# Performance work log

Measured on AMD Instinct MI355X. Metric: run time of the kernel, lower is better.

Reference implementation:

```python
import jax, jax.numpy as jnp
import numpy as np
from jax import lax

B0, H0, W0, C0 = 16, 32, 32, 512
D_ = C0 // 4      # per-group channels = d_inner (expand=1)
S = 1             # d_state
R = 8             # dt_rank = ceil(D_/16)


def layernorm(x, w, b, eps=1e-5):
    m = jnp.mean(x, axis=-1, keepdims=True)
    v = jnp.mean((x - m) ** 2, axis=-1, keepdims=True)
    return (x - m) / jnp.sqrt(v + eps) * w + b


def silu(x):
    return x * jax.nn.sigmoid(x)


def selective_scan(u, delta, A, Bs, Cs, Dp):
    # u,delta:(B,d,L)  A:(d,S)  Bs,Cs:(B,S,L)  Dp:(d,)
    a = jnp.exp(jnp.einsum('bdl,ds->bdsl', delta, A))      # decay per step
    bx = jnp.einsum('bdl,bsl,bdl->bdsl', delta, Bs, u)     # input injection
    def comb(c1, c2):
        a1, b1 = c1
        a2, b2 = c2
        return (a1 * a2, a2 * b1 + b2)
    _, h = lax.associative_scan(comb, (a, bx), axis=-1)    # h_t = a_t h_{t-1} + b_t
    return jnp.einsum('bdsl,bsl->bdl', h, Cs) + Dp[None, :, None] * u


def ss2d(xg, direction, ipw, cw, cb, xpw, dtw, dtb, Alog, Dp, onw, onb, opw):
    # xg: (B,H,W,dm); single-direction SS2D branch (CrossScan_i / CrossMerge_i)
    Bsz, Hh, Ww, dm = xg.shape
    xz = jnp.einsum('bhwc,oc->bhwo', xg, ipw)              # in_proj -> 2*d_inner
    xc, z = jnp.split(xz, 2, axis=-1)
    xc = xc.transpose(0, 3, 1, 2)                           # (B,d,H,W)
    xc = lax.conv_general_dilated(xc, cw, (1, 1), [(1, 1), (1, 1)],
                                  dimension_numbers=('NCHW', 'OIHW', 'NCHW'),
                                  feature_group_count=dm) + cb[None, :, None, None]
    xc = silu(xc)
    L = Hh * Ww
    if direction == 0:
        xs = xc.reshape(Bsz, dm, L)                         # row-major forward
    elif direction == 1:
        xs = xc.transpose(0, 1, 3, 2).reshape(Bsz, dm, L)   # column-major forward
    elif direction == 2:
        xs = xc.reshape(Bsz, dm, L)[:, :, ::-1]             # row-major reversed
    else:
        xs = xc.transpose(0, 1, 3, 2).reshape(Bsz, dm, L)[:, :, ::-1]
    xd = jnp.einsum('bdl,cd->bcl', xs, xpw)                 # x_proj -> (dt,B,C)
    dts, Bc, Cc = jnp.split(xd, [R, R + S], axis=1)
    delta = jax.nn.softplus(jnp.einsum('brl,dr->bdl', dts, dtw) + dtb[None, :, None])
    A = -jnp.exp(Alog)                                      # (d,S)
    y = selective_scan(xs, delta, A, Bc, Cc, Dp)
    if direction == 0:
        yhw = y.reshape(Bsz, dm, Hh, Ww)
    elif direction == 1:
        yhw = y.reshape(Bsz, dm, Ww, Hh).transpose(0, 1, 3, 2)
    elif direction == 2:
        yhw = y[:, :, ::-1].reshape(Bsz, dm, Hh, Ww)
    else:
        yhw = y[:, :, ::-1].reshape(Bsz, dm, Ww, Hh).transpose(0, 1, 3, 2)
    yo = yhw.transpose(0, 2, 3, 1)                          # (B,H,W,d)
    yo = layernorm(yo, onw, onb)
    yo = yo * silu(z)
    return jnp.einsum('bhwd,od->bhwo', yo, opw)             # out_proj


def setup_inputs() -> dict:
    key = jax.random.key(0)
    ks = jax.random.split(key, 12)
    def rn(k, shape, scale=0.02):
        return (jax.random.normal(k, shape) * scale).astype(jnp.float32)
    return dict(
        x=jax.random.normal(ks[0], (B0, H0 * W0, C0), dtype=jnp.float32),
        H=H0, W=W0,
        norm_w=jnp.ones((C0,), jnp.float32), norm_b=jnp.zeros((C0,), jnp.float32),
        fc_w=rn(ks[1], (C0, C0)), fc_b=jnp.zeros((C0,), jnp.float32),
        eca_w=rn(ks[2], (3,), 0.3),
        skip_scale=jnp.ones((), jnp.float32),
        proj_w=rn(ks[3], (C0, C0)), proj_b=jnp.zeros((C0,), jnp.float32),
        in_proj_w=rn(ks[4], (4, 2 * D_, D_)),
        conv_w=rn(ks[5], (4, D_, 1, 3, 3), 0.1), conv_b=jnp.zeros((4, D_), jnp.float32),
        x_proj_w=rn(ks[6], (4, R + 2 * S, D_)),
        dt_proj_w=rn(ks[7], (4, D_, R), 0.1), dt_proj_b=rn(ks[8], (4, D_), 0.1),
        A_log=jnp.zeros((4, D_, S), jnp.float32),           # A = -1 (d_state=1 init)
        D_param=jnp.ones((4, D_), jnp.float32),
        out_norm_w=jnp.ones((4, D_), jnp.float32), out_norm_b=jnp.zeros((4, D_), jnp.float32),
        out_proj_w=rn(ks[9], (4, D_, D_)),
    )


def reference(x, H, W, norm_w, norm_b, fc_w, fc_b, eca_w, skip_scale, proj_w, proj_b,
              in_proj_w, conv_w, conv_b, x_proj_w, dt_proj_w, dt_proj_b, A_log, D_param,
              out_norm_w, out_norm_b, out_proj_w):
    Bsz, N, Cc = x.shape
    xn = layernorm(x, norm_w, norm_b)
    # ECA-style channel gate: mean over tokens, 1D conv (k=3) over channel axis
    z_avg = jnp.mean(xn, axis=1)                            # (B,C)
    zp = jnp.pad(z_avg, ((0, 0), (1, 1)))
    y_eca = eca_w[0] * zp[:, :-2] + eca_w[1] * zp[:, 1:-1] + eca_w[2] * zp[:, 2:]
    gate = jax.nn.sigmoid(jnp.einsum('bc,oc->bo', z_avg, fc_w) + fc_b + y_eca)
    xh = xn.reshape(Bsz, H, W, Cc)
    groups = jnp.split(xh, 4, axis=-1)
    ys = []
    for g in range(4):                                      # 4 directional SS2D branches
        ys.append(ss2d(groups[g], g, in_proj_w[g], conv_w[g], conv_b[g], x_proj_w[g],
                       dt_proj_w[g], dt_proj_b[g], A_log[g], D_param[g],
                       out_norm_w[g], out_norm_b[g], out_proj_w[g]))
    xm = jnp.concatenate(ys, axis=-1) * skip_scale * xh
    xm = xm.reshape(Bsz, N, Cc) * gate[:, None, :]
    xm = layernorm(xm, norm_w, norm_b)
    return jnp.einsum('bnc,oc->bno', xm, proj_w) + proj_b
```

## Files before the change

kernel.cpp:

```cpp
#include <hip/hip_runtime.h>
#include <math.h>

#define NTOK 16384
#define NC 512
#define ND 128
#define NCH 64
#define CST 16

typedef __attribute__((ext_vector_type(8))) short bf16x8;
typedef __attribute__((ext_vector_type(4))) float f32x4;

#define LOG2E 1.4426950408889634f
#define LN2   0.6931471805599453f

__device__ __forceinline__ float fexp(float x){ return __builtin_amdgcn_exp2f(x * LOG2E); }
__device__ __forceinline__ float flog(float x){ return __builtin_amdgcn_logf(x) * LN2; }
__device__ __forceinline__ float sigf(float x){ return 1.f/(1.f + fexp(-x)); }

__device__ __forceinline__ float b2f(ushort u){ unsigned x = ((unsigned)u)<<16; return __builtin_bit_cast(float,x); }
__device__ __forceinline__ ushort f2b(float f){
  unsigned u = __builtin_bit_cast(unsigned,f);
  u += 0x7fff + ((u>>16)&1);
  return (ushort)(u>>16);
}

__device__ __forceinline__ int perm_pos(int g, int l){
  switch(g){
    case 0: return l;
    case 1: return ((l & 31) << 5) | (l >> 5);
    case 2: return 1023 - l;
    default:{ int ll = 1023 - l; return ((ll & 31) << 5) | (ll >> 5); }
  }
}

__device__ __forceinline__ void gload16(const void* g, void* l){
  __builtin_amdgcn_global_load_lds((const __attribute__((address_space(1))) void*)g,
                                   (__attribute__((address_space(3))) void*)l, 16, 0, 0);
}

__global__ __launch_bounds__(256) void k_tobf16_4(
    const float* __restrict__ s1, int n1, ushort* __restrict__ d1,
    const float* __restrict__ s2, int n2, ushort* __restrict__ d2,
    const float* __restrict__ s3, int n3, ushort* __restrict__ d3,
    const float* __restrict__ s4, int n4, ushort* __restrict__ d4){
  int i = blockIdx.x*256 + threadIdx.x;
  if (i < n1) d1[i] = f2b(s1[i]);
  else if (i < n1+n2) d2[i-n1] = f2b(s2[i-n1]);
  else if (i < n1+n2+n3) d3[i-n1-n2] = f2b(s3[i-n1-n2]);
  else if (i < n1+n2+n3+n4) d4[i-n1-n2-n3] = f2b(s4[i-n1-n2-n3]);
}

__global__ __launch_bounds__(256) void k_ln512(const float* __restrict__ x,
    const float* __restrict__ w, const float* __restrict__ b, ushort* __restrict__ out){
  int wv = threadIdx.x >> 6, lane = threadIdx.x & 63;
  int t = blockIdx.x*4 + wv;
  const float* xr = x + (size_t)t*NC + lane*8;
  float4 a = *(const float4*)xr;
  float4 c = *(const float4*)(xr+4);
  float e[8] = {a.x,a.y,a.z,a.w,c.x,c.y,c.z,c.w};
  float s = 0.f, sq = 0.f;
  #pragma unroll
  for (int i=0;i<8;i++){ s += e[i]; sq += e[i]*e[i]; }
  #pragma unroll
  for (int o=1;o<64;o<<=1){ s += __shfl_xor(s,o); sq += __shfl_xor(sq,o); }
  float m = s*(1.f/NC);
  float var = sq*(1.f/NC) - m*m;
  float rs = rsqrtf(var + 1e-5f);
  const float4* wr = (const float4*)(w + lane*8);
  const float4* br = (const float4*)(b + lane*8);
  float4 w0 = wr[0], w1 = wr[1], b0 = br[0], b1 = br[1];
  float wv8[8] = {w0.x,w0.y,w0.z,w0.w,w1.x,w1.y,w1.z,w1.w};
  float bv8[8] = {b0.x,b0.y,b0.z,b0.w,b1.x,b1.y,b1.z,b1.w};
  bf16x8 o8;
  #pragma unroll
  for (int i=0;i<8;i++) ((ushort*)&o8)[i] = f2b((e[i]-m)*rs*wv8[i]+bv8[i]);
  *(bf16x8*)(out + (size_t)t*NC + lane*8) = o8;
}

__global__ __launch_bounds__(512) void k_cm1(const ushort* __restrict__ xn,
    float* __restrict__ part){
  int c = threadIdx.x;
  const ushort* base = xn + ((size_t)blockIdx.x*32)*NC + c;
  float acc = 0.f;
  for (int n=0;n<32;n++) acc += b2f(base[(size_t)n*NC]);
  part[(size_t)blockIdx.x*NC + c] = acc;
}
__global__ __launch_bounds__(512) void k_cm2(const float* __restrict__ part,
    float* __restrict__ zavg){
  int b = blockIdx.x, c = threadIdx.x;
  float acc = 0.f;
  for (int i=0;i<32;i++) acc += part[(size_t)(b*32+i)*NC + c];
  zavg[b*NC+c] = acc * (1.f/1024.f);
}

__global__ __launch_bounds__(256) void k_gate(const float* __restrict__ zavg,
    const float* __restrict__ fcw, const float* __restrict__ fcb,
    const float* __restrict__ ew, float* __restrict__ gate){
  __shared__ float za[NC];
  int b = blockIdx.x >> 7, og = blockIdx.x & 127;
  int tid = threadIdx.x, lane = tid & 63, wv = tid >> 6;
  za[tid]     = zavg[b*NC + tid];
  za[tid+256] = zavg[b*NC + tid + 256];
  __syncthreads();
  int o = og*4 + wv;
  const float* wr = fcw + (size_t)o*NC;
  float acc = 0.f;
  #pragma unroll
  for (int i=0;i<8;i++) acc += za[lane + i*64]*wr[lane + i*64];
  #pragma unroll
  for (int off=1;off<64;off<<=1) acc += __shfl_xor(acc, off);
  if (lane==0){
    float left  = (o>0)    ? za[o-1] : 0.f;
    float right = (o<NC-1) ? za[o+1] : 0.f;
    float ye = ew[0]*left + ew[1]*za[o] + ew[2]*right;
    gate[b*NC+o] = sigf(acc + fcb[o] + ye);
  }
}

__global__ __launch_bounds__(256) void k_gemm_bf16(
    const ushort* __restrict__ A, int lda, long sAz,
    const ushort* __restrict__ Bw, int ldb, long sBz, int K,
    ushort* __restrict__ C0, int ldc0, ushort* __restrict__ C1, int ldc1,
    int nsplit, long sCz,
    float* __restrict__ Cf, int ldcf, const float* __restrict__ bias, int swz)
{
  __shared__ __align__(16) ushort Asm[128*64];
  __shared__ __align__(16) ushort Bsm[128*64];
  const int z = blockIdx.z;
  A  += (size_t)z*sAz;
  Bw += (size_t)z*sBz;
  if (C0) C0 += (size_t)z*sCz;
  if (C1) C1 += (size_t)z*sCz;
  int bx = blockIdx.x, by = blockIdx.y;
  if (swz){
    int nx = gridDim.x, nwg = nx * gridDim.y;
    int lin = by*nx + bx;
    int cpx = nwg >> 3;
    int s = (lin & 7)*cpx + (lin >> 3);
    bx = s % nx; by = s / nx;
  }
  const int tid = threadIdx.x;
  const int lane = tid & 63, wid = tid >> 6;
  const int wm = wid >> 1, wn = wid & 1;
  const int m0 = by * 128, n0 = bx * 128;

  const ushort* ga[4]; const ushort* gb[4]; int ldst[4];
  #pragma unroll
  for (int j=0;j<4;j++){
    int c = tid + 256*j;
    int r = c >> 3;
    int kb = ((c & 7) << 4) ^ ((r & 7) << 4);
    ga[j] = A  + (size_t)(m0 + r)*lda + (kb >> 1);
    gb[j] = Bw + (size_t)(n0 + r)*ldb + (kb >> 1);
    ldst[j] = c * 8;
  }

  f32x4 acc[4][4];
  #pragma unroll
  for (int i=0;i<4;i++)
    #pragma unroll
    for (int j=0;j<4;j++) acc[i][j] = (f32x4){0.f,0.f,0.f,0.f};

  const int lc = lane & 15;
  const int kgrp = (lane >> 4) << 4;

  for (int k0 = 0; k0 < K; k0 += 64){
    #pragma unroll
    for (int j=0;j<4;j++) gload16(ga[j] + k0, Asm + ldst[j]);
    #pragma unroll
    for (int j=0;j<4;j++) gload16(gb[j] + k0, Bsm + ldst[j]);
    __syncthreads();
    #pragma unroll
    for (int kk=0; kk<2; kk++){
      bf16x8 af[4], bfr[4];
      #pragma unroll
      for (int i=0;i<4;i++){
        int ra = wm*64 + i*16 + lc;
        int kb = kk*64 + kgrp;
        af[i] = *(const bf16x8*)((const char*)Asm + ra*128 + (kb ^ ((ra&7)<<4)));
        int rb = wn*64 + i*16 + lc;
        bfr[i] = *(const bf16x8*)((const char*)Bsm + rb*128 + (kb ^ ((rb&7)<<4)));
      }
      #pragma unroll
      for (int i=0;i<4;i++)
        #pragma unroll
        for (int j=0;j<4;j++)
          acc[i][j] = __builtin_amdgcn_mfma_f32_16x16x32_bf16(af[i], bfr[j], acc[i][j], 0, 0, 0);
    }
    __syncthreads();
  }

  const int lr = (lane >> 4) * 4;
  if (Cf){
    #pragma unroll
    for (int i=0;i<4;i++)
      #pragma unroll
      for (int j=0;j<4;j++){
        int row = m0 + wm*64 + i*16 + lr;
        int col = n0 + wn*64 + j*16 + lc;
        float bv = bias ? bias[col] : 0.f;
        #pragma unroll
        for (int r=0;r<4;r++)
          Cf[(size_t)(row+r)*ldcf + col] = acc[i][j][r] + bv;
      }
  } else {
    #pragma unroll
    for (int i=0;i<4;i++)
      #pragma unroll
      for (int j=0;j<4;j++){
        int row = m0 + wm*64 + i*16 + lr;
        int col = n0 + wn*64 + j*16 + lc;
        #pragma unroll
        for (int r=0;r<4;r++){
          ushort hv = f2b(acc[i][j][r]);
          if (col < nsplit) C0[(size_t)(row+r)*ldc0 + col] = hv;
          else              C1[(size_t)(row+r)*ldc1 + col - nsplit] = hv;
        }
      }
  }
}

__global__ __launch_bounds__(256) void k_convxp(const ushort* __restrict__ xc,
    const float* __restrict__ cw, const float* __restrict__ cb,
    const ushort* __restrict__ xpw_b, ushort* __restrict__ u, float* __restrict__ xd){
  __shared__ __align__(16) ushort xin[4*32*128];
  __shared__ __align__(16) ushort su[64][136];
  int g = blockIdx.z, tid = threadIdx.x;
  int blk = blockIdx.x;
  int bimg = blk >> 4, rp = blk & 15;
  int t0 = blk * 64;
  const ushort* xcg = xc + (size_t)g*NTOK*ND;

  #pragma unroll
  for (int j=0;j<8;j++){
    int c = tid + 256*j;
    int r = c >> 9;
    int rest = c & 511;
    int gr = 2*rp + r - 1;
    gr = min(max(gr, 0), 31);
    int w = rest >> 4, p = rest & 15;
    gload16(xcg + ((size_t)((bimg<<10) | (gr<<5) | w))*ND + p*8, (ushort*)xin + c*8);
  }

  int p = tid & 15, d0 = p*8;
  float w_[9][8]; float bias[8];
  {
    const float* wk = cw + (size_t)(g*ND + d0)*9;
    #pragma unroll
    for (int j=0;j<8;j++)
      #pragma unroll
      for (int k9=0;k9<9;k9++) w_[k9][j] = wk[j*9+k9];
    const float* cbp = cb + g*ND + d0;
    #pragma unroll
    for (int j=0;j<8;j++) bias[j] = cbp[j];
  }
  __syncthreads();

  #pragma unroll
  for (int pass=0; pass<4; pass++){
    int lt = pass*16 + (tid>>4);
    int hl = lt >> 5, w = lt & 31;
    int t = t0 + lt;
    float acc[8];
    #pragma unroll
    for (int j=0;j<8;j++) acc[j] = bias[j];
    #pragma unroll
    for (int kh=0;kh<3;kh++){
      int gr = 2*rp + hl + kh - 1;
      if (gr < 0 || gr >= 32) continue;
      #pragma unroll
      for (int kw=0;kw<3;kw++){
        int w2 = w + kw - 1;
        if (w2 < 0 || w2 >= 32) continue;
        bf16x8 v = *(const bf16x8*)&xin[((hl+kh)*32 + w2)*128 + d0];
        #pragma unroll
        for (int j=0;j<8;j++) acc[j] = fmaf(b2f(((ushort*)&v)[j]), w_[kh*3+kw][j], acc[j]);
      }
    }
    bf16x8 o8;
    #pragma unroll
    for (int j=0;j<8;j++){
      float uv = acc[j] * sigf(acc[j]);
      ((ushort*)&o8)[j] = f2b(uv);
    }
    *(bf16x8*)(u + ((size_t)g*NTOK + t)*ND + d0) = o8;
    *(bf16x8*)&su[lt][d0] = o8;
  }
  __syncthreads();

  int lane = tid & 63, wv = tid >> 6;
  int c = lane & 15;
  int kg = (lane >> 4) * 8;
  int cc = c < 10 ? c : 0;
  f32x4 acc4 = (f32x4){0.f,0.f,0.f,0.f};
  #pragma unroll
  for (int ks=0; ks<4; ks++){
    bf16x8 af = *(const bf16x8*)&su[wv*16 + (lane & 15)][ks*32 + kg];
    bf16x8 bfv = *(const bf16x8*)(xpw_b + (size_t)(g*10+cc)*128 + ks*32 + kg);
    if (c >= 10) bfv = (bf16x8){0,0,0,0,0,0,0,0};
    acc4 = __builtin_amdgcn_mfma_f32_16x16x32_bf16(af, bfv, acc4, 0, 0, 0);
  }
  if (c < 10){
    #pragma unroll
    for (int r=0;r<4;r++){
      int row = (lane >> 4)*4 + r;
      int t = t0 + wv*16 + row;
      xd[((size_t)g*NTOK + t)*12 + c] = acc4[r];
    }
  }
}

struct ScanCtx {
  float Ad, dtb_d;
  float w[8];
};

__device__ __forceinline__ void scan_step(const ScanCtx& c, float uv,
    const float4& x0, const float4& x1, float Bv,
    float& h, float& ap){
  float a = c.dtb_d;
  a = fmaf(x0.x, c.w[0], a); a = fmaf(x0.y, c.w[1], a);
  a = fmaf(x0.z, c.w[2], a); a = fmaf(x0.w, c.w[3], a);
  a = fmaf(x1.x, c.w[4], a); a = fmaf(x1.y, c.w[5], a);
  a = fmaf(x1.z, c.w[6], a); a = fmaf(x1.w, c.w[7], a);
  float dl = (a > 15.f) ? a : flog(1.f + fexp(a));
  float av = fexp(dl * c.Ad);
  h = fmaf(av, h, dl*Bv*uv);
  ap *= av;
}

__global__ __launch_bounds__(128) void k_scan1(const ushort* __restrict__ u,
    const float* __restrict__ xd, const float* __restrict__ Alog,
    const float* __restrict__ dtw, const float* __restrict__ dtb,
    float* __restrict__ chA, float* __restrict__ chB){
  int d = threadIdx.x, g = blockIdx.z;
  int b = blockIdx.x >> 6, ch = blockIdx.x & 63;
  ScanCtx c;
  c.Ad = -fexp(Alog[g*ND+d]);
  c.dtb_d = dtb[g*ND+d];
  const float4* wr = (const float4*)(dtw + (size_t)(g*ND+d)*8);
  float4 w0 = wr[0], w1 = wr[1];
  c.w[0]=w0.x;c.w[1]=w0.y;c.w[2]=w0.z;c.w[3]=w0.w;
  c.w[4]=w1.x;c.w[5]=w1.y;c.w[6]=w1.z;c.w[7]=w1.w;
  float h = 0.f, ap = 1.f;
  int l0 = ch*CST;
  #pragma unroll 4
  for (int s=0;s<CST;s++){
    int pp = perm_pos(g, l0 + s);
    size_t base = (size_t)g*NTOK + ((b<<10)|pp);
    float uv = b2f(u[base*ND + d]);
    const float4* xr = (const float4*)(xd + base*12);
    float4 x0 = xr[0], x1 = xr[1], x2 = xr[2];
    scan_step(c, uv, x0, x1, x2.x, h, ap);
  }
  size_t o = (((size_t)g*16 + b)*NCH + ch)*ND + d;
  chA[o]=ap; chB[o]=h;
}

__global__ __launch_bounds__(128) void k_scomb(const float* __restrict__ chA,
    const float* __restrict__ chB, float* __restrict__ hIn){
  int b = blockIdx.x, g = blockIdx.z, d = threadIdx.x;
  size_t base = (((size_t)g*16 + b)*NCH)*ND + d;
  float hrun = 0.f;
  #pragma unroll
  for (int ch=0; ch<NCH; ch++){
    size_t o = base + (size_t)ch*ND;
    float a = chA[o], bb = chB[o];
    hIn[o] = hrun;
    hrun = fmaf(a, hrun, bb);
  }
}

__global__ __launch_bounds__(128) void k_scan3(const ushort* __restrict__ u,
    const float* __restrict__ xd, const float* __restrict__ Alog,
    const float* __restrict__ dtw, const float* __restrict__ dtb,
    const float* __restrict__ Dp, const float* __restrict__ hIn,
    ushort* __restrict__ y){
  int d = threadIdx.x, g = blockIdx.z;
  int b = blockIdx.x >> 6, ch = blockIdx.x & 63;
  ScanCtx c;
  c.Ad = -fexp(Alog[g*ND+d]);
  c.dtb_d = dtb[g*ND+d];
  float Dd = Dp[g*ND+d];
  const float4* wr = (const float4*)(dtw + (size_t)(g*ND+d)*8);
  float4 w0 = wr[0], w1 = wr[1];
  c.w[0]=w0.x;c.w[1]=w0.y;c.w[2]=w0.z;c.w[3]=w0.w;
  c.w[4]=w1.x;c.w[5]=w1.y;c.w[6]=w1.z;c.w[7]=w1.w;
  float h = hIn[(((size_t)g*16 + b)*NCH + ch)*ND + d];
  float ap = 1.f;
  int l0 = ch*CST;
  #pragma unroll 4
  for (int s=0;s<CST;s++){
    int pp = perm_pos(g, l0 + s);
    size_t base = (size_t)g*NTOK + ((b<<10)|pp);
    float uv = b2f(u[base*ND + d]);
    const float4* xr = (const float4*)(xd + base*12);
    float4 x0 = xr[0], x1 = xr[1], x2 = xr[2];
    scan_step(c, uv, x0, x1, x2.x, h, ap);
    y[base*ND + d] = f2b(fmaf(h, x2.y, Dd*uv));
  }
}

__global__ __launch_bounds__(256) void k_yo(const ushort* __restrict__ y,
    const ushort* __restrict__ zg, const float* __restrict__ onw,
    const float* __restrict__ onb, ushort* __restrict__ yo){
  int tid = threadIdx.x, g = blockIdx.z;
  int lt = tid >> 4, p = tid & 15;
  int t = blockIdx.x*16 + lt;
  size_t base = ((size_t)g*NTOK + t)*ND + p*8;
  bf16x8 yv8 = *(const bf16x8*)(y + base);
  float e[8];
  float s = 0.f, sq = 0.f;
  #pragma unroll
  for (int i=0;i<8;i++){
    e[i] = b2f(((ushort*)&yv8)[i]);
    s += e[i]; sq += e[i]*e[i];
  }
  #pragma unroll
  for (int o=1;o<16;o<<=1){ s += __shfl_xor(s,o); sq += __shfl_xor(sq,o); }
  float m = s*(1.f/ND);
  float var = sq*(1.f/ND) - m*m;
  float rs = rsqrtf(var + 1e-5f);
  const float4* wr = (const float4*)(onw + g*ND + p*8);
  const float4* br = (const float4*)(onb + g*ND + p*8);
  float4 w0 = wr[0], w1 = wr[1], b0 = br[0], b1 = br[1];
  float wv8[8] = {w0.x,w0.y,w0.z,w0.w,w1.x,w1.y,w1.z,w1.w};
  float bv8[8] = {b0.x,b0.y,b0.z,b0.w,b1.x,b1.y,b1.z,b1.w};
  bf16x8 zv = *(const bf16x8*)(zg + base);
  bf16x8 o8;
  #pragma unroll
  for (int i=0;i<8;i++){
    float yn = (e[i]-m)*rs*wv8[i]+bv8[i];
    float z = b2f(((ushort*)&zv)[i]);
    ((ushort*)&o8)[i] = f2b(yn * z * sigf(z));
  }
  *(bf16x8*)(yo + base) = o8;
}

__global__ __launch_bounds__(256) void k_gateln(const ushort* __restrict__ ybuf,
    const ushort* __restrict__ xn, const float* __restrict__ gate,
    const float* __restrict__ skip, const float* __restrict__ w,
    const float* __restrict__ b, ushort* __restrict__ out){
  int wv = threadIdx.x >> 6, lane = threadIdx.x & 63;
  int t = blockIdx.x*4 + wv, bb = t >> 10;
  float ss = skip[0];
  size_t o0 = (size_t)t*NC + lane*8;
  bf16x8 yv = *(const bf16x8*)(ybuf + o0);
  bf16x8 xv = *(const bf16x8*)(xn + o0);
  const float4* gr = (const float4*)(gate + bb*NC + lane*8);
  float4 g0 = gr[0], g1 = gr[1];
  float gv8[8] = {g0.x,g0.y,g0.z,g0.w,g1.x,g1.y,g1.z,g1.w};
  float e[8];
  float s = 0.f, sq = 0.f;
  #pragma unroll
  for (int i=0;i<8;i++){
    e[i] = b2f(((ushort*)&yv)[i]) * ss * b2f(((ushort*)&xv)[i]) * gv8[i];
    s += e[i]; sq += e[i]*e[i];
  }
  #pragma unroll
  for (int o=1;o<64;o<<=1){ s += __shfl_xor(s,o); sq += __shfl_xor(sq,o); }
  float m = s*(1.f/NC);
  float var = sq*(1.f/NC) - m*m;
  float rs = rsqrtf(var + 1e-5f);
  const float4* wr = (const float4*)(w + lane*8);
  const float4* br = (const float4*)(b + lane*8);
  float4 w0 = wr[0], w1 = wr[1], b0 = br[0], b1 = br[1];
  float wv8[8] = {w0.x,w0.y,w0.z,w0.w,w1.x,w1.y,w1.z,w1.w};
  float bv8[8] = {b0.x,b0.y,b0.z,b0.w,b1.x,b1.y,b1.z,b1.w};
  bf16x8 o8;
  #pragma unroll
  for (int i=0;i<8;i++) ((ushort*)&o8)[i] = f2b((e[i]-m)*rs*wv8[i]+bv8[i]);
  *(bf16x8*)(out + o0) = o8;
}

extern "C" void kernel_launch(void* const* d_in, const int* in_sizes, int n_in,
                              void* d_out, int out_size, void* d_ws, size_t ws_size,
                              hipStream_t stream) {
  const float* x          = (const float*)d_in[0];
  const float* norm_w     = (const float*)d_in[3];
  const float* norm_b     = (const float*)d_in[4];
  const float* fc_w       = (const float*)d_in[5];
  const float* fc_b       = (const float*)d_in[6];
  const float* eca_w      = (const float*)d_in[7];
  const float* skip_scale = (const float*)d_in[8];
  const float* proj_w     = (const float*)d_in[9];
  const float* proj_b     = (const float*)d_in[10];
  const float* in_proj_w  = (const float*)d_in[11];
  const float* conv_w     = (const float*)d_in[12];
  const float* conv_b     = (const float*)d_in[13];
  const float* x_proj_w   = (const float*)d_in[14];
  const float* dt_proj_w  = (const float*)d_in[15];
  const float* dt_proj_b  = (const float*)d_in[16];
  const float* A_log      = (const float*)d_in[17];
  const float* D_param    = (const float*)d_in[18];
  const float* out_norm_w = (const float*)d_in[19];
  const float* out_norm_b = (const float*)d_in[20];
  const float* out_proj_w = (const float*)d_in[21];
  float* out = (float*)d_out;
  float* ws  = (float*)d_ws;

  ushort* xn_b   = (ushort*)(ws);
  ushort* ybuf_b = (ushort*)(ws + 4194304);
  ushort* xc4    = (ushort*)(ws + 8388608);
  ushort* zg4    = (ushort*)(ws + 12582912);
  ushort* yo4    = (ushort*)(ws + 16777216);
  ushort* u4b    = (ushort*)(ws + 20971520);
  ushort* y4b    = (ushort*)(ws + 25165824);
  float*  xd4    = ws + 29360128;
  float*  chA    = ws + 30146560;
  float*  chB    = ws + 30670848;
  float*  hIn    = ws + 31195136;
  float*  zavg   = ws + 31719424;
  float*  gatep  = ws + 31727616;
  float*  part   = ws + 31735808;
  ushort* wb_in  = (ushort*)(ws + 31997952);
  ushort* wb_out = (ushort*)(ws + 32063488);
  ushort* wb_prj = (ushort*)(ws + 32096256);
  ushort* wb_xp  = (ushort*)(ws + 32227328);
  ushort* xmn_b  = (ushort*)(ws + 32229888);

  k_ln512<<<dim3(NTOK/4), dim3(256), 0, stream>>>(x, norm_w, norm_b, xn_b);
  k_cm1<<<dim3(512), dim3(512), 0, stream>>>(xn_b, part);
  k_cm2<<<dim3(16), dim3(512), 0, stream>>>(part, zavg);
  k_gate<<<dim3(16*128), dim3(256), 0, stream>>>(zavg, fc_w, fc_b, eca_w, gatep);
  k_tobf16_4<<<dim3(1812), dim3(256), 0, stream>>>(
      in_proj_w, 131072, wb_in, out_proj_w, 65536, wb_out,
      proj_w, 262144, wb_prj, x_proj_w, 5120, wb_xp);

  k_gemm_bf16<<<dim3(2,128,4), dim3(256), 0, stream>>>(
      xn_b, NC, 128, wb_in, 128, 256*128, 128,
      xc4, 128, zg4, 128, 128, (long)NTOK*128,
      (float*)nullptr, 0, (const float*)nullptr, 0);

  k_convxp<<<dim3(NTOK/64,1,4), dim3(256), 0, stream>>>(
      xc4, conv_w, conv_b, wb_xp, u4b, xd4);

  k_scan1<<<dim3(16*NCH,1,4), dim3(128), 0, stream>>>(
      u4b, xd4, A_log, dt_proj_w, dt_proj_b, chA, chB);
  k_scomb<<<dim3(16,1,4), dim3(128), 0, stream>>>(chA, chB, hIn);
  k_scan3<<<dim3(16*NCH,1,4), dim3(128), 0, stream>>>(
      u4b, xd4, A_log, dt_proj_w, dt_proj_b, D_param, hIn, y4b);

  k_yo<<<dim3(NTOK/16,1,4), dim3(256), 0, stream>>>(
      y4b, zg4, out_norm_w, out_norm_b, yo4);

  k_gemm_bf16<<<dim3(1,128,4), dim3(256), 0, stream>>>(
      yo4, 128, (long)NTOK*128, wb_out, 128, 128*128, 128,
      ybuf_b, NC, ybuf_b, NC, 1<<30, 128,
      (float*)nullptr, 0, (const float*)nullptr, 0);

  k_gateln<<<dim3(NTOK/4), dim3(256), 0, stream>>>(
      ybuf_b, xn_b, gatep, skip_scale, norm_w, norm_b, xmn_b);

  k_gemm_bf16<<<dim3(4,128,1), dim3(256), 0, stream>>>(
      xmn_b, NC, 0, wb_prj, NC, 0, NC,
      (ushort*)nullptr, 0, (ushort*)nullptr, 0, 0, 0,
      out, NC, proj_b, 1);
}
```

Before: 136.4 us.

## Fold weight bf16 conversion into layernorm and chunk-combine into scan pass

The fp32-to-bf16 weight conversion now runs inside the first layernorm kernel, whose 4096 blocks cover the 464k converted elements. The separate chunk-prefix combine kernel is removed: each scan3 block serially folds all preceding chunk summaries (up to 63) to get its starting state. This drops two launches and the hIn buffer, but adds redundant prefix work in scan3 (quadratic total reads of chA/chB) and extra divergence in the layernorm kernel.

```diff
diff --git a/kernel.cpp b/kernel.cpp
--- a/kernel.cpp
+++ b/kernel.cpp
@@ -38,20 +38,18 @@
                                    (__attribute__((address_space(3))) void*)l, 16, 0, 0);
 }
 
-__global__ __launch_bounds__(256) void k_tobf16_4(
+__global__ __launch_bounds__(256) void k_ln512(const float* __restrict__ x,
+    const float* __restrict__ w, const float* __restrict__ b, ushort* __restrict__ out,
     const float* __restrict__ s1, int n1, ushort* __restrict__ d1,
     const float* __restrict__ s2, int n2, ushort* __restrict__ d2,
     const float* __restrict__ s3, int n3, ushort* __restrict__ d3,
     const float* __restrict__ s4, int n4, ushort* __restrict__ d4){
-  int i = blockIdx.x*256 + threadIdx.x;
-  if (i < n1) d1[i] = f2b(s1[i]);
-  else if (i < n1+n2) d2[i-n1] = f2b(s2[i-n1]);
-  else if (i < n1+n2+n3) d3[i-n1-n2] = f2b(s3[i-n1-n2]);
-  else if (i < n1+n2+n3+n4) d4[i-n1-n2-n3] = f2b(s4[i-n1-n2-n3]);
-}
-
-__global__ __launch_bounds__(256) void k_ln512(const float* __restrict__ x,
-    const float* __restrict__ w, const float* __restrict__ b, ushort* __restrict__ out){
+  int gidx = blockIdx.x*256 + threadIdx.x;
+  if (gidx < n1) d1[gidx] = f2b(s1[gidx]);
+  else if (gidx < n1+n2) d2[gidx-n1] = f2b(s2[gidx-n1]);
+  else if (gidx < n1+n2+n3) d3[gidx-n1-n2] = f2b(s3[gidx-n1-n2]);
+  else if (gidx < n1+n2+n3+n4) d4[gidx-n1-n2-n3] = f2b(s4[gidx-n1-n2-n3]);
+
   int wv = threadIdx.x >> 6, lane = threadIdx.x & 63;
   int t = blockIdx.x*4 + wv;
   const float* xr = x + (size_t)t*NC + lane*8;
@@ -315,18 +313,14 @@
   float w[8];
 };
 
-__device__ __forceinline__ void scan_step(const ScanCtx& c, float uv,
-    const float4& x0, const float4& x1, float Bv,
-    float& h, float& ap){
+__device__ __forceinline__ float delta_of(const ScanCtx& c,
+    const float4& x0, const float4& x1){
   float a = c.dtb_d;
   a = fmaf(x0.x, c.w[0], a); a = fmaf(x0.y, c.w[1], a);
   a = fmaf(x0.z, c.w[2], a); a = fmaf(x0.w, c.w[3], a);
   a = fmaf(x1.x, c.w[4], a); a = fmaf(x1.y, c.w[5], a);
   a = fmaf(x1.z, c.w[6], a); a = fmaf(x1.w, c.w[7], a);
-  float dl = (a > 15.f) ? a : flog(1.f + fexp(a));
-  float av = fexp(dl * c.Ad);
-  h = fmaf(av, h, dl*Bv*uv);
-  ap *= av;
+  return (a > 15.f) ? a : flog(1.f + fexp(a));
 }
 
 __global__ __launch_bounds__(128) void k_scan1(const ushort* __restrict__ u,
@@ -351,31 +345,20 @@
     float uv = b2f(u[base*ND + d]);
     const float4* xr = (const float4*)(xd + base*12);
     float4 x0 = xr[0], x1 = xr[1], x2 = xr[2];
-    scan_step(c, uv, x0, x1, x2.x, h, ap);
+    float dl = delta_of(c, x0, x1);
+    float av = fexp(dl * c.Ad);
+    h = fmaf(av, h, dl*x2.x*uv);
+    ap *= av;
   }
   size_t o = (((size_t)g*16 + b)*NCH + ch)*ND + d;
   chA[o]=ap; chB[o]=h;
-}
-
-__global__ __launch_bounds__(128) void k_scomb(const float* __restrict__ chA,
-    const float* __restrict__ chB, float* __restrict__ hIn){
-  int b = blockIdx.x, g = blockIdx.z, d = threadIdx.x;
-  size_t base = (((size_t)g*16 + b)*NCH)*ND + d;
-  float hrun = 0.f;
-  #pragma unroll
-  for (int ch=0; ch<NCH; ch++){
-    size_t o = base + (size_t)ch*ND;
-    float a = chA[o], bb = chB[o];
-    hIn[o] = hrun;
-    hrun = fmaf(a, hrun, bb);
-  }
 }
 
 __global__ __launch_bounds__(128) void k_scan3(const ushort* __restrict__ u,
     const float* __restrict__ xd, const float* __restrict__ Alog,
     const float* __restrict__ dtw, const float* __restrict__ dtb,
-    const float* __restrict__ Dp, const float* __restrict__ hIn,
-    ushort* __restrict__ y){
+    const float* __restrict__ Dp, const float* __restrict__ chA,
+    const float* __restrict__ chB, ushort* __restrict__ y){
   int d = threadIdx.x, g = blockIdx.z;
   int b = blockIdx.x >> 6, ch = blockIdx.x & 63;
   ScanCtx c;
@@ -386,8 +369,12 @@
   float4 w0 = wr[0], w1 = wr[1];
   c.w[0]=w0.x;c.w[1]=w0.y;c.w[2]=w0.z;c.w[3]=w0.w;
   c.w[4]=w1.x;c.w[5]=w1.y;c.w[6]=w1.z;c.w[7]=w1.w;
-  float h = hIn[(((size_t)g*16 + b)*NCH + ch)*ND + d];
-  float ap = 1.f;
+  size_t cbase = (((size_t)g*16 + b)*NCH)*ND + d;
+  float h = 0.f;
+  for (int k=0;k<ch;k++){
+    size_t o = cbase + (size_t)k*ND;
+    h = fmaf(chA[o], h, chB[o]);
+  }
   int l0 = ch*CST;
   #pragma unroll 4
   for (int s=0;s<CST;s++){
@@ -396,7 +383,9 @@
     float uv = b2f(u[base*ND + d]);
     const float4* xr = (const float4*)(xd + base*12);
     float4 x0 = xr[0], x1 = xr[1], x2 = xr[2];
-    scan_step(c, uv, x0, x1, x2.x, h, ap);
+    float dl = delta_of(c, x0, x1);
+    float av = fexp(dl * c.Ad);
+    h = fmaf(av, h, dl*x2.x*uv);
     y[base*ND + d] = f2b(fmaf(h, x2.y, Dd*uv));
   }
 }
@@ -509,7 +498,6 @@
   float*  xd4    = ws + 29360128;
   float*  chA    = ws + 30146560;
   float*  chB    = ws + 30670848;
-  float*  hIn    = ws + 31195136;
   float*  zavg   = ws + 31719424;
   float*  gatep  = ws + 31727616;
   float*  part   = ws + 31735808;
@@ -519,13 +507,12 @@
   ushort* wb_xp  = (ushort*)(ws + 32227328);
   ushort* xmn_b  = (ushort*)(ws + 32229888);
 
-  k_ln512<<<dim3(NTOK/4), dim3(256), 0, stream>>>(x, norm_w, norm_b, xn_b);
+  k_ln512<<<dim3(NTOK/4), dim3(256), 0, stream>>>(x, norm_w, norm_b, xn_b,
+      in_proj_w, 131072, wb_in, out_proj_w, 65536, wb_out,
+      proj_w, 262144, wb_prj, x_proj_w, 5120, wb_xp);
   k_cm1<<<dim3(512), dim3(512), 0, stream>>>(xn_b, part);
   k_cm2<<<dim3(16), dim3(512), 0, stream>>>(part, zavg);
   k_gate<<<dim3(16*128), dim3(256), 0, stream>>>(zavg, fc_w, fc_b, eca_w, gatep);
-  k_tobf16_4<<<dim3(1812), dim3(256), 0, stream>>>(
-      in_proj_w, 131072, wb_in, out_proj_w, 65536, wb_out,
-      proj_w, 262144, wb_prj, x_proj_w, 5120, wb_xp);
 
   k_gemm_bf16<<<dim3(2,128,4), dim3(256), 0, stream>>>(
       xn_b, NC, 128, wb_in, 128, 256*128, 128,
@@ -537,9 +524,8 @@
 
   k_scan1<<<dim3(16*NCH,1,4), dim3(128), 0, stream>>>(
       u4b, xd4, A_log, dt_proj_w, dt_proj_b, chA, chB);
-  k_scomb<<<dim3(16,1,4), dim3(128), 0, stream>>>(chA, chB, hIn);
   k_scan3<<<dim3(16*NCH,1,4), dim3(128), 0, stream>>>(
-      u4b, xd4, A_log, dt_proj_w, dt_proj_b, D_param, hIn, y4b);
+      u4b, xd4, A_log, dt_proj_w, dt_proj_b, D_param, chA, chB, y4b);
 
   k_yo<<<dim3(NTOK/16,1,4), dim3(256), 0, stream>>>(
       y4b, zg4, out_norm_w, out_norm_b, yo4);
```

After: 149.4 us. 9.5% more time.
